# Performance work log

Measured on AMD Instinct MI355X. Metric: run time of the kernel, lower is better.

The kernel has to match this reference:

```python
import jax, jax.numpy as jnp
import numpy as np

N, L = 131072, 4          # traffic lights, lanes per TL
E, H = 64, 128            # embed_dim, hidden_dim
NH, HD = 4, 16            # num_heads, head_dim (E = NH*HD)
NR, R = 4, 8              # num_regions, region_embed_dim
INIT_LOG_STD = -0.5


def _lin(k, fan_in, shape):
    b = 1.0 / np.sqrt(fan_in)
    return jax.random.uniform(k, shape, minval=-b, maxval=b, dtype=jnp.float32)


def setup_inputs() -> dict:
    key = jax.random.key(0)
    ks = jax.random.split(key, 32)
    inp = {
        "queue": jax.random.uniform(ks[0], (N, L), dtype=jnp.float32),
        "waiting": jax.random.uniform(ks[1], (N, L), dtype=jnp.float32),
        "phase_onehot": jax.random.uniform(ks[2], (N, 4), dtype=jnp.float32),
        "elapsed": jax.random.uniform(ks[3], (N,), dtype=jnp.float32),
        "region_ids": jax.random.randint(ks[4], (N,), 0, NR, dtype=jnp.int32),
        "noise": jax.random.normal(ks[5], (N,), dtype=jnp.float32),
        # lane_mlp: Linear(3,H) -> ReLU -> Linear(H,E) -> ReLU
        "lane_w1": _lin(ks[6], 3, (3, H)), "lane_b1": _lin(ks[7], 3, (H,)),
        "lane_w2": _lin(ks[8], H, (H, E)), "lane_b2": _lin(ks[9], H, (E,)),
        # MultiheadAttention in/out projections
        "attn_in_w": _lin(ks[10], E, (E, 3 * E)), "attn_in_b": jnp.zeros((3 * E,), jnp.float32),
        "attn_out_w": _lin(ks[11], E, (E, E)), "attn_out_b": jnp.zeros((E,), jnp.float32),
        # phase_mlp: Linear(5,H) -> ReLU -> Linear(H,H) -> ReLU
        "phase_w1": _lin(ks[12], 5, (5, H)), "phase_b1": _lin(ks[13], 5, (H,)),
        "phase_w2": _lin(ks[14], H, (H, H)), "phase_b2": _lin(ks[15], H, (H,)),
        # region embedding table
        "region_table": jax.random.normal(ks[16], (NR, R), dtype=jnp.float32),
        # mlp_head: Linear(E+H+R, H) -> ReLU -> Linear(H, 1)
        "head_w1": _lin(ks[17], E + H + R, (E + H + R, H)), "head_b1": _lin(ks[18], E + H + R, (H,)),
        "head_w2": _lin(ks[19], H, (H, 1)), "head_b2": _lin(ks[20], H, (1,)),
        "log_std": jnp.full((1,), INIT_LOG_STD, dtype=jnp.float32),
    }
    return inp


def reference(queue, waiting, phase_onehot, elapsed, region_ids, noise,
              lane_w1, lane_b1, lane_w2, lane_b2,
              attn_in_w, attn_in_b, attn_out_w, attn_out_b,
              phase_w1, phase_b1, phase_w2, phase_b2,
              region_table, head_w1, head_b1, head_w2, head_b2, log_std):
    # --- lane context: tiny MLP + self-attention over L lanes, batched over N TLs ---
    lane_feats = jnp.stack([queue, waiting, jnp.broadcast_to(elapsed[:, None], (N, L))], axis=-1)  # [N,L,3]
    h = jax.nn.relu(lane_feats @ lane_w1 + lane_b1)          # [N,L,H]
    emb = jax.nn.relu(h @ lane_w2 + lane_b2)                 # [N,L,E]

    qkv = emb @ attn_in_w + attn_in_b                        # [N,L,3E]
    q, k, v = jnp.split(qkv, 3, axis=-1)
    def heads(x):  # [N,L,E] -> [N,NH,L,HD]
        return x.reshape(N, L, NH, HD).transpose(0, 2, 1, 3)
    q, k, v = heads(q), heads(k), heads(v)
    scores = jnp.einsum('bhqd,bhkd->bhqk', q, k) / np.sqrt(HD)   # [N,NH,L,L]
    attn = jax.nn.softmax(scores, axis=-1)
    o = jnp.einsum('bhqk,bhkd->bhqd', attn, v)               # [N,NH,L,HD]
    o = o.transpose(0, 2, 1, 3).reshape(N, L, E)
    attn_out = o @ attn_out_w + attn_out_b                   # [N,L,E]
    ctx = attn_out.mean(axis=1)                              # [N,E]

    # --- phase MLP ---
    phase_elapsed = jnp.concatenate([phase_onehot, elapsed[:, None]], axis=-1)  # [N,5]
    ph = jax.nn.relu(phase_elapsed @ phase_w1 + phase_b1)
    phase_emb = jax.nn.relu(ph @ phase_w2 + phase_b2)        # [N,H]

    # --- region embedding (clamped index) ---
    rid = jnp.clip(region_ids, 0, NR - 1)
    region_emb = region_table[rid]                           # [N,R]

    # --- Gaussian head ---
    feat = jnp.concatenate([ctx, phase_emb, region_emb], axis=-1)  # [N,E+H+R]
    means = (jax.nn.relu(feat @ head_w1 + head_b1) @ head_w2 + head_b2)[:, 0]  # [N]

    ls = jnp.broadcast_to(log_std, means.shape)
    std = jnp.exp(ls)
    actions = means + std * noise
    actions_clamped = jnp.clip(actions, -1.0, 1.0)
    log_prob = -0.5 * ((actions - means) ** 2 / (std * std) + 2.0 * ls + np.log(2.0 * np.pi))
    return actions_clamped, log_prob
```

## Files before the change

### kernel.cpp

```cpp
#include <hip/hip_runtime.h>
#include <math.h>

#define N_TL 131072
#define GRID 2048
#define BLK 256

#define NFRAG 70
#define WS_CONST_OFF (NFRAG * 256)
#define NCONST 1346

typedef __attribute__((ext_vector_type(8))) short bfrag;
typedef __attribute__((ext_vector_type(4))) float f32x4;
typedef __attribute__((ext_vector_type(16))) float f32x16;

__device__ __forceinline__ unsigned short f2bf_rne(float x) {
  unsigned int u = __float_as_uint(x);
  return (unsigned short)((u + 0x7fffu + ((u >> 16) & 1u)) >> 16);
}
__device__ __forceinline__ unsigned int pack2(float a, float b) {
  return __builtin_amdgcn_perm(__float_as_uint(b) + 0x8000u,
                               __float_as_uint(a) + 0x8000u, 0x07060302u);
}
__device__ __forceinline__ float lo16(unsigned int u) { return __uint_as_float(u << 16); }
__device__ __forceinline__ float hi16(unsigned int u) { return __uint_as_float(u & 0xffff0000u); }
__device__ __forceinline__ f32x4 mfma16(bfrag a, bfrag b, f32x4 c) {
  return __builtin_amdgcn_mfma_f32_16x16x32_bf16(a, b, c, 0, 0, 0);
}
__device__ __forceinline__ f32x16 mfma32(bfrag a, bfrag b, f32x16 c) {
  return __builtin_amdgcn_mfma_f32_32x32x16_bf16(a, b, c, 0, 0, 0);
}

__device__ __forceinline__ bfrag load_wfragT(const float* __restrict__ w, int ncols,
                                             int col0, int k0, int lane, int K, float scale) {
  const int mm = lane & 15, qq = lane >> 4;
  bfrag f;
  #pragma unroll
  for (int j = 0; j < 8; ++j) {
    const int k = k0 + qq * 8 + j;
    const float v = (k < K) ? w[(size_t)k * ncols + col0 + mm] * scale : 0.f;
    f[j] = (short)f2bf_rne(v);
  }
  return f;
}
__device__ __forceinline__ bfrag load_wfragT32(const float* __restrict__ w, int ncols,
                                               int m0, int k0, int lane, int K, float scale) {
  const int mm = lane & 31, q1 = lane >> 5;
  bfrag f;
  #pragma unroll
  for (int j = 0; j < 8; ++j) {
    const int k = k0 + q1 * 8 + j;
    const float v = (k < K) ? w[(size_t)k * ncols + m0 + mm] * scale : 0.f;
    f[j] = (short)f2bf_rne(v);
  }
  return f;
}

__device__ __forceinline__ bfrag ldfrag(const uint4* __restrict__ WF, int f, int tid) {
  uint4 u = WF[f * 256 + tid];
  return *reinterpret_cast<bfrag*>(&u);
}

__device__ __forceinline__ bfrag ldb32f(const unsigned short* arr, int stride, int row,
                                        int kk, int q1) {
  return *reinterpret_cast<const bfrag*>(&arr[row * stride + kk * 16 + q1 * 8]);
}
__device__ __forceinline__ f32x16 binit32(const float* bias, int chBase, int q1) {
  f32x16 a;
  #pragma unroll
  for (int g = 0; g < 4; ++g) {
    const f32x4 bb = *reinterpret_cast<const f32x4*>(&bias[chBase + g * 8 + q1 * 4]);
    a[g * 4 + 0] = bb[0]; a[g * 4 + 1] = bb[1];
    a[g * 4 + 2] = bb[2]; a[g * 4 + 3] = bb[3];
  }
  return a;
}
__device__ __forceinline__ void st32(unsigned short* arr, int stride, int row,
                                     int chBase, int q1, f32x16 acc, bool relu) {
  #pragma unroll
  for (int g = 0; g < 4; ++g) {
    float a0 = acc[g * 4 + 0], a1 = acc[g * 4 + 1];
    float a2 = acc[g * 4 + 2], a3 = acc[g * 4 + 3];
    if (relu) {
      a0 = fmaxf(a0, 0.f); a1 = fmaxf(a1, 0.f);
      a2 = fmaxf(a2, 0.f); a3 = fmaxf(a3, 0.f);
    }
    uint2 u;
    u.x = pack2(a0, a1);
    u.y = pack2(a2, a3);
    *reinterpret_cast<uint2*>(&arr[row * stride + chBase + g * 8 + q1 * 4]) = u;
  }
}

#define LDBACT(arr, stride, nt, kk) \
  (*reinterpret_cast<const bfrag*>(&(arr)[((nt) * 16 + m) * (stride) + (kk) * 32 + quad * 8]))

__global__ __launch_bounds__(BLK)
void prep_weights(const float* __restrict__ lane_w1, const float* __restrict__ lane_b1,
                  const float* __restrict__ lane_w2, const float* __restrict__ lane_b2,
                  const float* __restrict__ attn_in_w, const float* __restrict__ attn_in_b,
                  const float* __restrict__ attn_out_w, const float* __restrict__ attn_out_b,
                  const float* __restrict__ phase_w1, const float* __restrict__ phase_b1,
                  const float* __restrict__ phase_w2, const float* __restrict__ phase_b2,
                  const float* __restrict__ region_table,
                  const float* __restrict__ head_w1, const float* __restrict__ head_b1,
                  const float* __restrict__ head_w2, const float* __restrict__ head_b2,
                  const float* __restrict__ log_std,
                  uint4* __restrict__ ws) {
  const int f = blockIdx.x;
  const int tid = threadIdx.x;
  const int wv = tid >> 6, lane = tid & 63;
  const int mb = wv >> 1;
  bfrag r;
  if (f < 8) {
    r = load_wfragT32(lane_w2, 64, mb * 32, f * 16, lane, 128, 1.f);
  } else if (f < 20) {
    const int t = (f - 8) >> 2, kk = (f - 8) & 3;
    r = load_wfragT32(attn_in_w, 192, (mb + 2 * t) * 32, kk * 16, lane, 64,
                      t == 0 ? 0.25f : 1.f);
  } else if (f < 22) {
    r = load_wfragT(attn_out_w, 64, wv * 16, (f - 20) * 32, lane, 64, 0.25f);
  } else if (f < 26) {
    const int t = (f - 22) >> 1, kk = (f - 22) & 1;
    r = load_wfragT32(lane_w1, 128, (mb + 2 * t) * 32, kk * 16, lane, 3, 1.f);
  } else if (f < 30) {
    const int t = (f - 26) >> 1, kk = (f - 26) & 1;
    r = load_wfragT32(phase_w1, 128, (mb + 2 * t) * 32, kk * 16, lane, 5, 1.f);
  } else if (f < 46) {
    const int t = (f - 30) >> 3, kk = (f - 30) & 7;
    r = load_wfragT32(phase_w2, 128, (mb + 2 * t) * 32, kk * 16, lane, 128, 1.f);
  } else {
    const int t = (f - 46) / 12, kk = (f - 46) % 12;
    r = load_wfragT32(head_w1, 128, (mb + 2 * t) * 32, kk * 16, lane, 192, 1.f);
  }
  ws[f * 256 + tid] = *reinterpret_cast<uint4*>(&r);

  if (f == 0) {
    float* wc = reinterpret_cast<float*>(ws + WS_CONST_OFF);
    for (int i = tid; i < NCONST; i += BLK) {
      float v;
      if (i < 128)       v = lane_b1[i];
      else if (i < 192)  v = lane_b2[i - 128];
      else if (i < 384)  { const int j = i - 192; v = attn_in_b[j] * ((j < 64) ? 0.25f : 1.f); }
      else if (i < 448)  v = attn_out_b[i - 384];
      else if (i < 576)  v = phase_b1[i - 448];
      else if (i < 704)  v = phase_b2[i - 576];
      else if (i < 1216) {
        const int g = (i - 704) >> 7, c = (i - 704) & 127;
        float a = head_b1[c];
        #pragma unroll
        for (int j = 0; j < 8; ++j) a += region_table[g * 8 + j] * head_w1[(192 + j) * 128 + c];
        v = a;
      }
      else if (i < 1344) v = head_w2[i - 1216];
      else if (i == 1344) v = head_b2[0];
      else               v = log_std[0];
      wc[i] = v;
    }
  }
}

struct alignas(16) SmemF {
  union {
    unsigned short qkv[64 * 200];
    unsigned short h[64 * 136];
    unsigned short ph[64 * 136];
  };
  unsigned short emb[64 * 72];
  unsigned short xbuf[64 * 40];
  unsigned short feat[64 * 200];
  float b1[128], b2[64], bin[192], bout[64];
  float pb1[128], pb2[128];
  float rbias[4][128];
  float hw2[128];
  float consts[2];
  int ridx[64];
};

__global__ __launch_bounds__(BLK, 2)
void fused_policy(const float* __restrict__ queue,
                  const float* __restrict__ waiting,
                  const float* __restrict__ phase_onehot,
                  const float* __restrict__ elapsed,
                  const int* __restrict__ region_ids,
                  const float* __restrict__ noise,
                  const uint4* __restrict__ WF,
                  float* __restrict__ out) {
  __shared__ SmemF S;
  const int tid  = threadIdx.x;
  const int wv   = tid >> 6;
  const int lane = tid & 63;
  const int m    = lane & 15;
  const int quad = lane >> 4;
  const int n32  = lane & 31;
  const int q1   = lane >> 5;
  const int mb   = wv >> 1;
  const int row64 = (wv & 1) * 32 + n32;
  const int n0   = blockIdx.x * 64;

  bfrag wL1[2][2], wL2[8], wQKV[3][4], wOUT2[2];
  #pragma unroll
  for (int kk = 0; kk < 8; ++kk) wL2[kk] = ldfrag(WF, kk, tid);
  #pragma unroll
  for (int t = 0; t < 3; ++t)
    #pragma unroll
    for (int kk = 0; kk < 4; ++kk) wQKV[t][kk] = ldfrag(WF, 8 + t * 4 + kk, tid);
  #pragma unroll
  for (int kk = 0; kk < 2; ++kk) wOUT2[kk] = ldfrag(WF, 20 + kk, tid);
  #pragma unroll
  for (int t = 0; t < 2; ++t)
    #pragma unroll
    for (int kk = 0; kk < 2; ++kk) wL1[t][kk] = ldfrag(WF, 22 + t * 2 + kk, tid);

  {
    const float2* src = reinterpret_cast<const float2*>(WF + WS_CONST_OFF);
    float2* dst = reinterpret_cast<float2*>(&S.b1[0]);
    for (int i = tid; i < NCONST / 2; i += BLK) dst[i] = src[i];
  }
  if (tid < 64) {
    int r = region_ids[n0 + tid];
    S.ridx[tid] = r < 0 ? 0 : (r > 3 ? 3 : r);
  }
  {
    const int r = tid >> 2, seg = tid & 3;
    uint4 z = {0, 0, 0, 0};
    if (seg == 0) {
      const int gl = n0 * 4 + r;
      z.x = pack2(queue[gl], waiting[gl]);
      z.y = pack2(elapsed[n0 + (r >> 2)], 0.f);
    }
    *reinterpret_cast<uint4*>(&S.xbuf[r * 40 + seg * 8]) = z;
  }
  __syncthreads();

  #pragma unroll 1
  for (int s = 0; s < 4; ++s) {
    const int tl0 = n0 + s * 16;

    {
      f32x16 acc[2];
      #pragma unroll
      for (int t = 0; t < 2; ++t) acc[t] = binit32(S.b1, (mb + 2 * t) * 32, q1);
      #pragma unroll
      for (int kk = 0; kk < 2; ++kk) {
        const bfrag b = ldb32f(S.xbuf, 40, row64, kk, q1);
        acc[0] = mfma32(wL1[0][kk], b, acc[0]);
        acc[1] = mfma32(wL1[1][kk], b, acc[1]);
      }
      #pragma unroll
      for (int t = 0; t < 2; ++t) st32(S.h, 136, row64, (mb + 2 * t) * 32, q1, acc[t], true);
    }
    __syncthreads();

    {
      f32x16 acc = binit32(S.b2, mb * 32, q1);
      #pragma unroll
      for (int kk = 0; kk < 8; ++kk)
        acc = mfma32(wL2[kk], ldb32f(S.h, 136, row64, kk, q1), acc);
      st32(S.emb, 72, row64, mb * 32, q1, acc, true);
    }
    __syncthreads();

    {
      f32x16 acc[3];
      #pragma unroll
      for (int t = 0; t < 3; ++t) acc[t] = binit32(S.bin, (mb + 2 * t) * 32, q1);
      #pragma unroll
      for (int kk = 0; kk < 4; ++kk) {
        const bfrag b = ldb32f(S.emb, 72, row64, kk, q1);
        #pragma unroll
        for (int t = 0; t < 3; ++t) acc[t] = mfma32(wQKV[t][kk], b, acc[t]);
      }
      #pragma unroll
      for (int t = 0; t < 3; ++t)
        st32(S.qkv, 200, row64, (mb + 2 * t) * 32, q1, acc[t], false);

      const int r = tid >> 2, seg = tid & 3;
      uint4 z = {0, 0, 0, 0};
      if (s < 3) {
        if (seg == 0) {
          const int gl = (tl0 + 16) * 4 + r;
          z.x = pack2(queue[gl], waiting[gl]);
          z.y = pack2(elapsed[tl0 + 16 + (r >> 2)], 0.f);
        }
      } else {
        if (seg == 0) {
          const float4 p = *reinterpret_cast<const float4*>(&phase_onehot[(n0 + r) * 4]);
          z.x = pack2(p.x, p.y);
          z.y = pack2(p.z, p.w);
          z.z = pack2(elapsed[n0 + r], 0.f);
        }
      }
      *reinterpret_cast<uint4*>(&S.xbuf[r * 40 + seg * 8]) = z;
    }
    __syncthreads();

    {
      const int tl = tid >> 4, l16 = tid & 15;
      const int hh = l16 >> 2, lq = l16 & 3;
      const uint4* qp = reinterpret_cast<const uint4*>(
          &S.qkv[(tl * 4 + lq) * 200 + hh * 16]);
      const uint4 qA = qp[0], qB = qp[1];
      const unsigned int qu[8] = {qA.x, qA.y, qA.z, qA.w, qB.x, qB.y, qB.z, qB.w};
      float qlo[8], qhi[8];
      #pragma unroll
      for (int j = 0; j < 8; ++j) { qlo[j] = lo16(qu[j]); qhi[j] = hi16(qu[j]); }
      float sc[4];
      #pragma unroll
      for (int lk = 0; lk < 4; ++lk) {
        const uint4* kp = reinterpret_cast<const uint4*>(
            &S.qkv[(tl * 4 + lk) * 200 + 64 + hh * 16]);
        const uint4 kA = kp[0], kB = kp[1];
        const unsigned int ku[8] = {kA.x, kA.y, kA.z, kA.w, kB.x, kB.y, kB.z, kB.w};
        float tx = 0.f, ty = 0.f;
        #pragma unroll
        for (int j = 0; j < 8; ++j) {
          tx += qlo[j] * lo16(ku[j]);
          ty += qhi[j] * hi16(ku[j]);
        }
        sc[lk] = tx + ty;
      }
      const float mx = fmaxf(fmaxf(sc[0], sc[1]), fmaxf(sc[2], sc[3]));
      const float e0 = __expf(sc[0] - mx), e1 = __expf(sc[1] - mx);
      const float e2 = __expf(sc[2] - mx), e3 = __expf(sc[3] - mx);
      const float inv = 1.f / (e0 + e1 + e2 + e3);
      const float pr[4] = {e0 * inv, e1 * inv, e2 * inv, e3 * inv};
      float olo[8], ohi[8];
      #pragma unroll
      for (int j = 0; j < 8; ++j) { olo[j] = 0.f; ohi[j] = 0.f; }
      #pragma unroll
      for (int lk = 0; lk < 4; ++lk) {
        const uint4* vp = reinterpret_cast<const uint4*>(
            &S.qkv[(tl * 4 + lk) * 200 + 128 + hh * 16]);
        const uint4 vA = vp[0], vB = vp[1];
        const unsigned int vu[8] = {vA.x, vA.y, vA.z, vA.w, vB.x, vB.y, vB.z, vB.w};
        const float p = pr[lk];
        #pragma unroll
        for (int j = 0; j < 8; ++j) {
          olo[j] += p * lo16(vu[j]);
          ohi[j] += p * hi16(vu[j]);
        }
      }
      unsigned short* om = S.emb;
      const int base = tl * 264 + lq * 64 + hh * 16;
      *reinterpret_cast<uint4*>(&om[base]) =
          make_uint4(pack2(olo[0], ohi[0]), pack2(olo[1], ohi[1]),
                     pack2(olo[2], ohi[2]), pack2(olo[3], ohi[3]));
      *reinterpret_cast<uint4*>(&om[base + 8]) =
          make_uint4(pack2(olo[4], ohi[4]), pack2(olo[5], ohi[5]),
                     pack2(olo[6], ohi[6]), pack2(olo[7], ohi[7]));
    }
    __syncthreads();

    {
      const int oc0 = wv * 16 + quad * 4;
      f32x4 acc = *reinterpret_cast<const f32x4*>(&S.bout[oc0]);
      #pragma unroll
      for (int kk = 0; kk < 8; ++kk)
        acc = mfma16(wOUT2[kk & 1], LDBACT(S.emb, 264, 0, kk), acc);
      uint2 u;
      u.x = pack2(acc[0], acc[1]);
      u.y = pack2(acc[2], acc[3]);
      *reinterpret_cast<uint2*>(&S.feat[(s * 16 + m) * 200 + oc0]) = u;
    }
  }
  __syncthreads();

  __builtin_amdgcn_sched_barrier(0);
  bfrag wP1[2][2], wP2[2][8], wH1[2][12];
  #pragma unroll
  for (int t = 0; t < 2; ++t) {
    #pragma unroll
    for (int kk = 0; kk < 2; ++kk)  wP1[t][kk] = ldfrag(WF, 26 + t * 2 + kk, tid);
    #pragma unroll
    for (int kk = 0; kk < 8; ++kk)  wP2[t][kk] = ldfrag(WF, 30 + t * 8 + kk, tid);
    #pragma unroll
    for (int kk = 0; kk < 12; ++kk) wH1[t][kk] = ldfrag(WF, 46 + t * 12 + kk, tid);
  }

  {
    f32x16 acc[2];
    #pragma unroll
    for (int t = 0; t < 2; ++t) acc[t] = binit32(S.pb1, (mb + 2 * t) * 32, q1);
    #pragma unroll
    for (int kk = 0; kk < 2; ++kk) {
      const bfrag b = ldb32f(S.xbuf, 40, row64, kk, q1);
      acc[0] = mfma32(wP1[0][kk], b, acc[0]);
      acc[1] = mfma32(wP1[1][kk], b, acc[1]);
    }
    #pragma unroll
    for (int t = 0; t < 2; ++t) st32(S.ph, 136, row64, (mb + 2 * t) * 32, q1, acc[t], true);
  }
  __syncthreads();

  {
    f32x16 acc[2];
    #pragma unroll
    for (int t = 0; t < 2; ++t) acc[t] = binit32(S.pb2, (mb + 2 * t) * 32, q1);
    #pragma unroll
    for (int kk = 0; kk < 8; ++kk) {
      const bfrag b = ldb32f(S.ph, 136, row64, kk, q1);
      acc[0] = mfma32(wP2[0][kk], b, acc[0]);
      acc[1] = mfma32(wP2[1][kk], b, acc[1]);
    }
    #pragma unroll
    for (int t = 0; t < 2; ++t)
      st32(S.feat, 200, row64, 64 + (mb + 2 * t) * 32, q1, acc[t], true);
  }
  __syncthreads();

  {
    const int g = S.ridx[row64];
    f32x16 acc[2];
    #pragma unroll
    for (int t = 0; t < 2; ++t) acc[t] = binit32(S.rbias[g], (mb + 2 * t) * 32, q1);
    #pragma unroll
    for (int kk = 0; kk < 12; ++kk) {
      const bfrag b = ldb32f(S.feat, 200, row64, kk, q1);
      acc[0] = mfma32(wH1[0][kk], b, acc[0]);
      acc[1] = mfma32(wH1[1][kk], b, acc[1]);
    }
    #pragma unroll
    for (int t = 0; t < 2; ++t) st32(S.ph, 136, row64, (mb + 2 * t) * 32, q1, acc[t], true);
  }
  __syncthreads();

  {
    const int tl = tid >> 2, s4 = tid & 3;
    const uint4* hp = reinterpret_cast<const uint4*>(&S.ph[tl * 136 + s4 * 32]);
    const uint4 h0 = hp[0], h1 = hp[1], h2 = hp[2], h3 = hp[3];
    const unsigned int hu[16] = {h0.x, h0.y, h0.z, h0.w, h1.x, h1.y, h1.z, h1.w,
                                 h2.x, h2.y, h2.z, h2.w, h3.x, h3.y, h3.z, h3.w};
    float t = 0.f;
    #pragma unroll
    for (int j = 0; j < 16; ++j) {
      t += lo16(hu[j]) * S.hw2[s4 * 32 + 2 * j];
      t += hi16(hu[j]) * S.hw2[s4 * 32 + 2 * j + 1];
    }
    t += __shfl_xor(t, 1);
    t += __shfl_xor(t, 2);
    if (s4 == 0) {
      const int n = n0 + tl;
      const float means = t + S.consts[0];
      const float ls = S.consts[1];
      const float nz = noise[n];
      const float a = means + __expf(ls) * nz;
      out[n] = fminf(fmaxf(a, -1.f), 1.f);
      out[N_TL + n] = -0.5f * (nz * nz + 2.f * ls + 1.8378770664093453f);
    }
  }
}

extern "C" void kernel_launch(void* const* d_in, const int* in_sizes, int n_in,
                              void* d_out, int out_size, void* d_ws, size_t ws_size,
                              hipStream_t stream) {
  const float* queue        = (const float*)d_in[0];
  const float* waiting      = (const float*)d_in[1];
  const float* phase_onehot = (const float*)d_in[2];
  const float* elapsed      = (const float*)d_in[3];
  const int*   region_ids   = (const int*)d_in[4];
  const float* noise        = (const float*)d_in[5];
  const float* lane_w1      = (const float*)d_in[6];
  const float* lane_b1      = (const float*)d_in[7];
  const float* lane_w2      = (const float*)d_in[8];
  const float* lane_b2      = (const float*)d_in[9];
  const float* attn_in_w    = (const float*)d_in[10];
  const float* attn_in_b    = (const float*)d_in[11];
  const float* attn_out_w   = (const float*)d_in[12];
  const float* attn_out_b   = (const float*)d_in[13];
  const float* phase_w1     = (const float*)d_in[14];
  const float* phase_b1     = (const float*)d_in[15];
  const float* phase_w2     = (const float*)d_in[16];
  const float* phase_b2     = (const float*)d_in[17];
  const float* region_table = (const float*)d_in[18];
  const float* head_w1      = (const float*)d_in[19];
  const float* head_b1      = (const float*)d_in[20];
  const float* head_w2      = (const float*)d_in[21];
  const float* head_b2      = (const float*)d_in[22];
  const float* log_std      = (const float*)d_in[23];

  float* out = (float*)d_out;
  uint4* ws  = (uint4*)d_ws;
  (void)ws_size;

  hipLaunchKernelGGL(prep_weights, dim3(NFRAG), dim3(BLK), 0, stream,
                     lane_w1, lane_b1, lane_w2, lane_b2,
                     attn_in_w, attn_in_b, attn_out_w, attn_out_b,
                     phase_w1, phase_b1, phase_w2, phase_b2, region_table,
                     head_w1, head_b1, head_w2, head_b2, log_std, ws);

  hipLaunchKernelGGL(fused_policy, dim3(GRID), dim3(BLK), 0, stream,
                     queue, waiting, phase_onehot, elapsed, region_ids, noise,
                     (const uint4*)ws, out);
}
```

Before: 191.0 us.

## Halve per-block tile to 32 lights, reshape weight fragments for 4 blocks/CU

New measurement: 183.4 us. 4.0% less time.

```diff
diff --git a/kernel.cpp b/kernel.cpp
--- a/kernel.cpp
+++ b/kernel.cpp
@@ -2,10 +2,10 @@
 #include <math.h>
 
 #define N_TL 131072
-#define GRID 2048
+#define GRID 4096
 #define BLK 256
 
-#define NFRAG 70
+#define NFRAG 36
 #define WS_CONST_OFF (NFRAG * 256)
 #define NCONST 1346
 
@@ -109,28 +109,23 @@
   const int f = blockIdx.x;
   const int tid = threadIdx.x;
   const int wv = tid >> 6, lane = tid & 63;
-  const int mb = wv >> 1;
   bfrag r;
-  if (f < 8) {
-    r = load_wfragT32(lane_w2, 64, mb * 32, f * 16, lane, 128, 1.f);
-  } else if (f < 20) {
-    const int t = (f - 8) >> 2, kk = (f - 8) & 3;
-    r = load_wfragT32(attn_in_w, 192, (mb + 2 * t) * 32, kk * 16, lane, 64,
-                      t == 0 ? 0.25f : 1.f);
-  } else if (f < 22) {
-    r = load_wfragT(attn_out_w, 64, wv * 16, (f - 20) * 32, lane, 64, 0.25f);
-  } else if (f < 26) {
-    const int t = (f - 22) >> 1, kk = (f - 22) & 1;
-    r = load_wfragT32(lane_w1, 128, (mb + 2 * t) * 32, kk * 16, lane, 3, 1.f);
-  } else if (f < 30) {
-    const int t = (f - 26) >> 1, kk = (f - 26) & 1;
-    r = load_wfragT32(phase_w1, 128, (mb + 2 * t) * 32, kk * 16, lane, 5, 1.f);
-  } else if (f < 46) {
-    const int t = (f - 30) >> 3, kk = (f - 30) & 7;
-    r = load_wfragT32(phase_w2, 128, (mb + 2 * t) * 32, kk * 16, lane, 128, 1.f);
+  if (f < 4) {
+    r = load_wfragT(lane_w2, 64, wv * 16, f * 32, lane, 128, 1.f);
+  } else if (f < 10) {
+    const int t = (f - 4) >> 1, kk = (f - 4) & 1;
+    r = load_wfragT(attn_in_w, 192, (wv + t * 4) * 16, kk * 32, lane, 64,
+                    t == 0 ? 0.25f : 1.f);
+  } else if (f < 12) {
+    r = load_wfragT(attn_out_w, 64, wv * 16, (f - 10) * 32, lane, 64, 0.25f);
+  } else if (f < 14) {
+    r = load_wfragT32(lane_w1, 128, wv * 32, (f - 12) * 16, lane, 3, 1.f);
+  } else if (f < 16) {
+    r = load_wfragT32(phase_w1, 128, wv * 32, (f - 14) * 16, lane, 5, 1.f);
+  } else if (f < 24) {
+    r = load_wfragT32(phase_w2, 128, wv * 32, (f - 16) * 16, lane, 128, 1.f);
   } else {
-    const int t = (f - 46) / 12, kk = (f - 46) % 12;
-    r = load_wfragT32(head_w1, 128, (mb + 2 * t) * 32, kk * 16, lane, 192, 1.f);
+    r = load_wfragT32(head_w1, 128, wv * 32, (f - 24) * 16, lane, 192, 1.f);
   }
   ws[f * 256 + tid] = *reinterpret_cast<uint4*>(&r);
 
@@ -161,22 +156,22 @@
 
 struct alignas(16) SmemF {
   union {
-    unsigned short qkv[64 * 200];
-    unsigned short h[64 * 136];
-    unsigned short ph[64 * 136];
+    unsigned short qkv[32 * 200];
+    unsigned short h[32 * 136];
+    unsigned short ph[32 * 136];
   };
-  unsigned short emb[64 * 72];
-  unsigned short xbuf[64 * 40];
-  unsigned short feat[64 * 200];
+  unsigned short emb[32 * 72];
+  unsigned short xbuf[32 * 40];
+  unsigned short feat[32 * 200];
   float b1[128], b2[64], bin[192], bout[64];
   float pb1[128], pb2[128];
   float rbias[4][128];
   float hw2[128];
   float consts[2];
-  int ridx[64];
+  int ridx[32];
 };
 
-__global__ __launch_bounds__(BLK, 2)
+__global__ __launch_bounds__(BLK, 4)
 void fused_policy(const float* __restrict__ queue,
                   const float* __restrict__ waiting,
                   const float* __restrict__ phase_onehot,
@@ -193,161 +188,183 @@
   const int quad = lane >> 4;
   const int n32  = lane & 31;
   const int q1   = lane >> 5;
-  const int mb   = wv >> 1;
-  const int row64 = (wv & 1) * 32 + n32;
-  const int n0   = blockIdx.x * 64;
-
-  bfrag wL1[2][2], wL2[8], wQKV[3][4], wOUT2[2];
-  #pragma unroll
-  for (int kk = 0; kk < 8; ++kk) wL2[kk] = ldfrag(WF, kk, tid);
+  const int n0   = blockIdx.x * 32;
+
+  bfrag wL1[2], wL2[4], wQKV[3][2], wOUT2[2];
+  #pragma unroll
+  for (int kk = 0; kk < 4; ++kk) wL2[kk] = ldfrag(WF, kk, tid);
   #pragma unroll
   for (int t = 0; t < 3; ++t)
     #pragma unroll
-    for (int kk = 0; kk < 4; ++kk) wQKV[t][kk] = ldfrag(WF, 8 + t * 4 + kk, tid);
-  #pragma unroll
-  for (int kk = 0; kk < 2; ++kk) wOUT2[kk] = ldfrag(WF, 20 + kk, tid);
-  #pragma unroll
-  for (int t = 0; t < 2; ++t)
-    #pragma unroll
-    for (int kk = 0; kk < 2; ++kk) wL1[t][kk] = ldfrag(WF, 22 + t * 2 + kk, tid);
+    for (int kk = 0; kk < 2; ++kk) wQKV[t][kk] = ldfrag(WF, 4 + t * 2 + kk, tid);
+  #pragma unroll
+  for (int kk = 0; kk < 2; ++kk) wOUT2[kk] = ldfrag(WF, 10 + kk, tid);
+  #pragma unroll
+  for (int kk = 0; kk < 2; ++kk) wL1[kk] = ldfrag(WF, 12 + kk, tid);
 
   {
     const float2* src = reinterpret_cast<const float2*>(WF + WS_CONST_OFF);
     float2* dst = reinterpret_cast<float2*>(&S.b1[0]);
     for (int i = tid; i < NCONST / 2; i += BLK) dst[i] = src[i];
   }
-  if (tid < 64) {
+  if (tid < 32) {
     int r = region_ids[n0 + tid];
     S.ridx[tid] = r < 0 ? 0 : (r > 3 ? 3 : r);
   }
   {
     const int r = tid >> 2, seg = tid & 3;
-    uint4 z = {0, 0, 0, 0};
-    if (seg == 0) {
-      const int gl = n0 * 4 + r;
-      z.x = pack2(queue[gl], waiting[gl]);
-      z.y = pack2(elapsed[n0 + (r >> 2)], 0.f);
-    }
-    *reinterpret_cast<uint4*>(&S.xbuf[r * 40 + seg * 8]) = z;
+    if (r < 32) {
+      uint4 z = {0, 0, 0, 0};
+      if (seg == 0) {
+        const int gl = n0 * 4 + r;
+        z.x = pack2(queue[gl], waiting[gl]);
+        z.y = pack2(elapsed[n0 + (r >> 2)], 0.f);
+      }
+      *reinterpret_cast<uint4*>(&S.xbuf[r * 40 + seg * 8]) = z;
+    }
   }
   __syncthreads();
 
   #pragma unroll 1
   for (int s = 0; s < 4; ++s) {
-    const int tl0 = n0 + s * 16;
+    const int tl0 = n0 + s * 8;
 
     {
-      f32x16 acc[2];
-      #pragma unroll
-      for (int t = 0; t < 2; ++t) acc[t] = binit32(S.b1, (mb + 2 * t) * 32, q1);
-      #pragma unroll
-      for (int kk = 0; kk < 2; ++kk) {
-        const bfrag b = ldb32f(S.xbuf, 40, row64, kk, q1);
-        acc[0] = mfma32(wL1[0][kk], b, acc[0]);
-        acc[1] = mfma32(wL1[1][kk], b, acc[1]);
-      }
-      #pragma unroll
-      for (int t = 0; t < 2; ++t) st32(S.h, 136, row64, (mb + 2 * t) * 32, q1, acc[t], true);
+      f32x16 acc = binit32(S.b1, wv * 32, q1);
+      #pragma unroll
+      for (int kk = 0; kk < 2; ++kk)
+        acc = mfma32(wL1[kk], ldb32f(S.xbuf, 40, n32, kk, q1), acc);
+      st32(S.h, 136, n32, wv * 32, q1, acc, true);
     }
     __syncthreads();
 
     {
-      f32x16 acc = binit32(S.b2, mb * 32, q1);
-      #pragma unroll
-      for (int kk = 0; kk < 8; ++kk)
-        acc = mfma32(wL2[kk], ldb32f(S.h, 136, row64, kk, q1), acc);
-      st32(S.emb, 72, row64, mb * 32, q1, acc, true);
+      const int oc0 = wv * 16 + quad * 4;
+      const f32x4 bb = *reinterpret_cast<const f32x4*>(&S.b2[oc0]);
+      f32x4 acc[2] = {bb, bb};
+      #pragma unroll
+      for (int Nt = 0; Nt < 2; ++Nt)
+        #pragma unroll
+        for (int kk = 0; kk < 4; ++kk)
+          acc[Nt] = mfma16(wL2[kk], LDBACT(S.h, 136, Nt, kk), acc[Nt]);
+      #pragma unroll
+      for (int Nt = 0; Nt < 2; ++Nt) {
+        const int row = Nt * 16 + m;
+        uint2 u;
+        u.x = pack2(fmaxf(acc[Nt][0], 0.f), fmaxf(acc[Nt][1], 0.f));
+        u.y = pack2(fmaxf(acc[Nt][2], 0.f), fmaxf(acc[Nt][3], 0.f));
+        *reinterpret_cast<uint2*>(&S.emb[row * 72 + oc0]) = u;
+      }
     }
     __syncthreads();
 
     {
-      f32x16 acc[3];
-      #pragma unroll
-      for (int t = 0; t < 3; ++t) acc[t] = binit32(S.bin, (mb + 2 * t) * 32, q1);
-      #pragma unroll
-      for (int kk = 0; kk < 4; ++kk) {
-        const bfrag b = ldb32f(S.emb, 72, row64, kk, q1);
-        #pragma unroll
-        for (int t = 0; t < 3; ++t) acc[t] = mfma32(wQKV[t][kk], b, acc[t]);
-      }
-      #pragma unroll
-      for (int t = 0; t < 3; ++t)
-        st32(S.qkv, 200, row64, (mb + 2 * t) * 32, q1, acc[t], false);
-
+      f32x4 acc[3][2];
+      #pragma unroll
+      for (int t = 0; t < 3; ++t) {
+        const f32x4 bb = *reinterpret_cast<const f32x4*>(&S.bin[(wv + t * 4) * 16 + quad * 4]);
+        acc[t][0] = bb; acc[t][1] = bb;
+      }
+      #pragma unroll
+      for (int Nt = 0; Nt < 2; ++Nt) {
+        const bfrag e0 = LDBACT(S.emb, 72, Nt, 0);
+        const bfrag e1 = LDBACT(S.emb, 72, Nt, 1);
+        #pragma unroll
+        for (int t = 0; t < 3; ++t) {
+          acc[t][Nt] = mfma16(wQKV[t][0], e0, acc[t][Nt]);
+          acc[t][Nt] = mfma16(wQKV[t][1], e1, acc[t][Nt]);
+        }
+      }
+      #pragma unroll
+      for (int t = 0; t < 3; ++t) {
+        const int oc0 = (wv + t * 4) * 16 + quad * 4;
+        #pragma unroll
+        for (int Nt = 0; Nt < 2; ++Nt) {
+          const int row = Nt * 16 + m;
+          uint2 u;
+          u.x = pack2(acc[t][Nt][0], acc[t][Nt][1]);
+          u.y = pack2(acc[t][Nt][2], acc[t][Nt][3]);
+          *reinterpret_cast<uint2*>(&S.qkv[row * 200 + oc0]) = u;
+        }
+      }
       const int r = tid >> 2, seg = tid & 3;
-      uint4 z = {0, 0, 0, 0};
-      if (s < 3) {
-        if (seg == 0) {
-          const int gl = (tl0 + 16) * 4 + r;
-          z.x = pack2(queue[gl], waiting[gl]);
-          z.y = pack2(elapsed[tl0 + 16 + (r >> 2)], 0.f);
+      if (r < 32) {
+        uint4 z = {0, 0, 0, 0};
+        if (s < 3) {
+          if (seg == 0) {
+            const int gl = (tl0 + 8) * 4 + r;
+            z.x = pack2(queue[gl], waiting[gl]);
+            z.y = pack2(elapsed[tl0 + 8 + (r >> 2)], 0.f);
+          }
+        } else {
+          if (seg == 0) {
+            const float4 p = *reinterpret_cast<const float4*>(&phase_onehot[(n0 + r) * 4]);
+            z.x = pack2(p.x, p.y);
+            z.y = pack2(p.z, p.w);
+            z.z = pack2(elapsed[n0 + r], 0.f);
+          }
         }
-      } else {
-        if (seg == 0) {
-          const float4 p = *reinterpret_cast<const float4*>(&phase_onehot[(n0 + r) * 4]);
-          z.x = pack2(p.x, p.y);
-          z.y = pack2(p.z, p.w);
-          z.z = pack2(elapsed[n0 + r], 0.f);
-        }
-      }
-      *reinterpret_cast<uint4*>(&S.xbuf[r * 40 + seg * 8]) = z;
+        *reinterpret_cast<uint4*>(&S.xbuf[r * 40 + seg * 8]) = z;
+      }
     }
     __syncthreads();
 
     {
       const int tl = tid >> 4, l16 = tid & 15;
-      const int hh = l16 >> 2, lq = l16 & 3;
-      const uint4* qp = reinterpret_cast<const uint4*>(
-          &S.qkv[(tl * 4 + lq) * 200 + hh * 16]);
-      const uint4 qA = qp[0], qB = qp[1];
-      const unsigned int qu[8] = {qA.x, qA.y, qA.z, qA.w, qB.x, qB.y, qB.z, qB.w};
-      float qlo[8], qhi[8];
-      #pragma unroll
-      for (int j = 0; j < 8; ++j) { qlo[j] = lo16(qu[j]); qhi[j] = hi16(qu[j]); }
-      float sc[4];
-      #pragma unroll
-      for (int lk = 0; lk < 4; ++lk) {
-        const uint4* kp = reinterpret_cast<const uint4*>(
-            &S.qkv[(tl * 4 + lk) * 200 + 64 + hh * 16]);
-        const uint4 kA = kp[0], kB = kp[1];
-        const unsigned int ku[8] = {kA.x, kA.y, kA.z, kA.w, kB.x, kB.y, kB.z, kB.w};
-        float tx = 0.f, ty = 0.f;
-        #pragma unroll
-        for (int j = 0; j < 8; ++j) {
-          tx += qlo[j] * lo16(ku[j]);
-          ty += qhi[j] * hi16(ku[j]);
+      if (tl < 8) {
+        const int hh = l16 >> 2, lq = l16 & 3;
+        const uint4* qp = reinterpret_cast<const uint4*>(
+            &S.qkv[(tl * 4 + lq) * 200 + hh * 16]);
+        const uint4 qA = qp[0], qB = qp[1];
+        const unsigned int qu[8] = {qA.x, qA.y, qA.z, qA.w, qB.x, qB.y, qB.z, qB.w};
+        float qlo[8], qhi[8];
+        #pragma unroll
+        for (int j = 0; j < 8; ++j) { qlo[j] = lo16(qu[j]); qhi[j] = hi16(qu[j]); }
+        float sc[4];
+        #pragma unroll
+        for (int lk = 0; lk < 4; ++lk) {
+          const uint4* kp = reinterpret_cast<const uint4*>(
+              &S.qkv[(tl * 4 + lk) * 200 + 64 + hh * 16]);
+          const uint4 kA = kp[0], kB = kp[1];
+          const unsigned int ku[8] = {kA.x, kA.y, kA.z, kA.w, kB.x, kB.y, kB.z, kB.w};
+          float tx = 0.f, ty = 0.f;
+          #pragma unroll
+          for (int j = 0; j < 8; ++j) {
+            tx += qlo[j] * lo16(ku[j]);
+            ty += qhi[j] * hi16(ku[j]);
+          }
+          sc[lk] = tx + ty;
         }
-        sc[lk] = tx + ty;
-      }
-      const float mx = fmaxf(fmaxf(sc[0], sc[1]), fmaxf(sc[2], sc[3]));
-      const float e0 = __expf(sc[0] - mx), e1 = __expf(sc[1] - mx);
-      const float e2 = __expf(sc[2] - mx), e3 = __expf(sc[3] - mx);
-      const float inv = 1.f / (e0 + e1 + e2 + e3);
-      const float pr[4] = {e0 * inv, e1 * inv, e2 * inv, e3 * inv};
-      float olo[8], ohi[8];
-      #pragma unroll
-      for (int j = 0; j < 8; ++j) { olo[j] = 0.f; ohi[j] = 0.f; }
-      #pragma unroll
-      for (int lk = 0; lk < 4; ++lk) {
-        const uint4* vp = reinterpret_cast<const uint4*>(
-            &S.qkv[(tl * 4 + lk) * 200 + 128 + hh * 16]);
-        const uint4 vA = vp[0], vB = vp[1];
-        const unsigned int vu[8] = {vA.x, vA.y, vA.z, vA.w, vB.x, vB.y, vB.z, vB.w};
-        const float p = pr[lk];
-        #pragma unroll
-        for (int j = 0; j < 8; ++j) {
-          olo[j] += p * lo16(vu[j]);
-          ohi[j] += p * hi16(vu[j]);
+        const float mx = fmaxf(fmaxf(sc[0], sc[1]), fmaxf(sc[2], sc[3]));
+        const float e0 = __expf(sc[0] - mx), e1 = __expf(sc[1] - mx);
+        const float e2 = __expf(sc[2] - mx), e3 = __expf(sc[3] - mx);
+        const float inv = 1.f / (e0 + e1 + e2 + e3);
+        const float pr[4] = {e0 * inv, e1 * inv, e2 * inv, e3 * inv};
+        float olo[8], ohi[8];
+        #pragma unroll
+        for (int j = 0; j < 8; ++j) { olo[j] = 0.f; ohi[j] = 0.f; }
+        #pragma unroll
+        for (int lk = 0; lk < 4; ++lk) {
+          const uint4* vp = reinterpret_cast<const uint4*>(
+              &S.qkv[(tl * 4 + lk) * 200 + 128 + hh * 16]);
+          const uint4 vA = vp[0], vB = vp[1];
+          const unsigned int vu[8] = {vA.x, vA.y, vA.z, vA.w, vB.x, vB.y, vB.z, vB.w};
+          const float p = pr[lk];
+          #pragma unroll
+          for (int j = 0; j < 8; ++j) {
+            olo[j] += p * lo16(vu[j]);
+            ohi[j] += p * hi16(vu[j]);
+          }
         }
-      }
-      unsigned short* om = S.emb;
-      const int base = tl * 264 + lq * 64 + hh * 16;
-      *reinterpret_cast<uint4*>(&om[base]) =
-          make_uint4(pack2(olo[0], ohi[0]), pack2(olo[1], ohi[1]),
-                     pack2(olo[2], ohi[2]), pack2(olo[3], ohi[3]));
-      *reinterpret_cast<uint4*>(&om[base + 8]) =
-          make_uint4(pack2(olo[4], ohi[4]), pack2(olo[5], ohi[5]),
-                     pack2(olo[6], ohi[6]), pack2(olo[7], ohi[7]));
+        unsigned short* om = S.emb;
+        const int base = tl * 264 + lq * 64 + hh * 16;
+        *reinterpret_cast<uint4*>(&om[base]) =
+            make_uint4(pack2(olo[0], ohi[0]), pack2(olo[1], ohi[1]),
+                       pack2(olo[2], ohi[2]), pack2(olo[3], ohi[3]));
+        *reinterpret_cast<uint4*>(&om[base + 8]) =
+            make_uint4(pack2(olo[4], ohi[4]), pack2(olo[5], ohi[5]),
+                       pack2(olo[6], ohi[6]), pack2(olo[7], ohi[7]));
+      }
     }
     __syncthreads();
 
@@ -357,74 +374,55 @@
       #pragma unroll
       for (int kk = 0; kk < 8; ++kk)
         acc = mfma16(wOUT2[kk & 1], LDBACT(S.emb, 264, 0, kk), acc);
-      uint2 u;
-      u.x = pack2(acc[0], acc[1]);
-      u.y = pack2(acc[2], acc[3]);
-      *reinterpret_cast<uint2*>(&S.feat[(s * 16 + m) * 200 + oc0]) = u;
+      if (m < 8) {
+        uint2 u;
+        u.x = pack2(acc[0], acc[1]);
+        u.y = pack2(acc[2], acc[3]);
+        *reinterpret_cast<uint2*>(&S.feat[(s * 8 + m) * 200 + oc0]) = u;
+      }
     }
   }
   __syncthreads();
-
   __builtin_amdgcn_sched_barrier(0);
-  bfrag wP1[2][2], wP2[2][8], wH1[2][12];
-  #pragma unroll
-  for (int t = 0; t < 2; ++t) {
-    #pragma unroll
-    for (int kk = 0; kk < 2; ++kk)  wP1[t][kk] = ldfrag(WF, 26 + t * 2 + kk, tid);
-    #pragma unroll
-    for (int kk = 0; kk < 8; ++kk)  wP2[t][kk] = ldfrag(WF, 30 + t * 8 + kk, tid);
-    #pragma unroll
-    for (int kk = 0; kk < 12; ++kk) wH1[t][kk] = ldfrag(WF, 46 + t * 12 + kk, tid);
-  }
 
   {
-    f32x16 acc[2];
-    #pragma unroll
-    for (int t = 0; t < 2; ++t) acc[t] = binit32(S.pb1, (mb + 2 * t) * 32, q1);
-    #pragma unroll
-    for (int kk = 0; kk < 2; ++kk) {
-      const bfrag b = ldb32f(S.xbuf, 40, row64, kk, q1);
-      acc[0] = mfma32(wP1[0][kk], b, acc[0]);
-      acc[1] = mfma32(wP1[1][kk], b, acc[1]);
-    }
-    #pragma unroll
-    for (int t = 0; t < 2; ++t) st32(S.ph, 136, row64, (mb + 2 * t) * 32, q1, acc[t], true);
+    bfrag wP1[2];
+    #pragma unroll
+    for (int kk = 0; kk < 2; ++kk) wP1[kk] = ldfrag(WF, 14 + kk, tid);
+    f32x16 acc = binit32(S.pb1, wv * 32, q1);
+    #pragma unroll
+    for (int kk = 0; kk < 2; ++kk)
+      acc = mfma32(wP1[kk], ldb32f(S.xbuf, 40, n32, kk, q1), acc);
+    st32(S.ph, 136, n32, wv * 32, q1, acc, true);
   }
   __syncthreads();
 
   {
-    f32x16 acc[2];
-    #pragma unroll
-    for (int t = 0; t < 2; ++t) acc[t] = binit32(S.pb2, (mb + 2 * t) * 32, q1);
-    #pragma unroll
-    for (int kk = 0; kk < 8; ++kk) {
-      const bfrag b = ldb32f(S.ph, 136, row64, kk, q1);
-      acc[0] = mfma32(wP2[0][kk], b, acc[0]);
-      acc[1] = mfma32(wP2[1][kk], b, acc[1]);
-    }
-    #pragma unroll
-    for (int t = 0; t < 2; ++t)
-      st32(S.feat, 200, row64, 64 + (mb + 2 * t) * 32, q1, acc[t], true);
+    bfrag wP2[8];
+    #pragma unroll
+    for (int kk = 0; kk < 8; ++kk) wP2[kk] = ldfrag(WF, 16 + kk, tid);
+    f32x16 acc = binit32(S.pb2, wv * 32, q1);
+    #pragma unroll
+    for (int kk = 0; kk < 8; ++kk)
+      acc = mfma32(wP2[kk], ldb32f(S.ph, 136, n32, kk, q1), acc);
+    st32(S.feat, 200, n32, 64 + wv * 32, q1, acc, true);
   }
   __syncthreads();
 
   {
-    const int g = S.ridx[row64];
-    f32x16 acc[2];
-    #pragma unroll
-    for (int t = 0; t < 2; ++t) acc[t] = binit32(S.rbias[g], (mb + 2 * t) * 32, q1);
-    #pragma unroll
-    for (int kk = 0; kk < 12; ++kk) {
-      const bfrag b = ldb32f(S.feat, 200, row64, kk, q1);
-      acc[0] = mfma32(wH1[0][kk], b, acc[0]);
-      acc[1] = mfma32(wH1[1][kk], b, acc[1]);
-    }
-    #pragma unroll
-    for (int t = 0; t < 2; ++t) st32(S.ph, 136, row64, (mb + 2 * t) * 32, q1, acc[t], true);
+    bfrag wH1[12];
+    #pragma unroll
+    for (int kk = 0; kk < 12; ++kk) wH1[kk] = ldfrag(WF, 24 + kk, tid);
+    const int g = S.ridx[n32];
+    f32x16 acc = binit32(S.rbias[g], wv * 32, q1);
+    #pragma unroll
+    for (int kk = 0; kk < 12; ++kk)
+      acc = mfma32(wH1[kk], ldb32f(S.feat, 200, n32, kk, q1), acc);
+    st32(S.ph, 136, n32, wv * 32, q1, acc, true);
   }
   __syncthreads();
 
-  {
+  if (tid < 128) {
     const int tl = tid >> 2, s4 = tid & 3;
     const uint4* hp = reinterpret_cast<const uint4*>(&S.ph[tl * 136 + s4 * 32]);
     const uint4 h0 = hp[0], h1 = hp[1], h2 = hp[2], h3 = hp[3];
```
